# Kernel tuning notes

Measured on AMD Instinct MI355X. Metric: run time of the kernel, lower is better.

The kernel has to match this reference:

```python
import jax, jax.numpy as jnp
import numpy as np

B, C, H, W = 4, 256, 64, 64
DQ = C // 8

def setup_inputs() -> dict:
    key = jax.random.key(0)
    ks = jax.random.split(key, 7)
    x = jax.random.normal(ks[0], (B, C, H, W), dtype=jnp.float32)
    # 1x1 convs == per-pixel linear layers: weight [out, in], bias [out]
    Wq = jax.random.normal(ks[1], (DQ, C), dtype=jnp.float32) * (1.0 / np.sqrt(C))
    bq = jax.random.normal(ks[2], (DQ,), dtype=jnp.float32) * 0.01
    Wk = jax.random.normal(ks[3], (DQ, C), dtype=jnp.float32) * (1.0 / np.sqrt(C))
    bk = jax.random.normal(ks[4], (DQ,), dtype=jnp.float32) * 0.01
    Wv = jax.random.normal(ks[5], (C, C), dtype=jnp.float32) * (1.0 / np.sqrt(C))
    bv = jax.random.normal(ks[6], (C,), dtype=jnp.float32) * 0.01
    return {"x": x, "Wq": Wq, "bq": bq, "Wk": Wk, "bk": bk, "Wv": Wv, "bv": bv}

def reference(x, Wq, bq, Wk, bk, Wv, bv):
    b, c, h, w = x.shape
    n = h * w
    xf = x.reshape(b, c, n)                                  # [b,c,n]
    Q = jnp.einsum('dc,bcn->bnd', Wq, xf) + bq               # [b,n,dq]
    K = jnp.einsum('dc,bcn->bdn', Wk, xf) + bk[None, :, None]  # [b,dq,n]
    A = jax.nn.softmax(jnp.einsum('bnd,bdm->bnm', Q, K), axis=-1)  # [b,n,n]
    V = jnp.einsum('oc,bcn->bon', Wv, xf) + bv[None, :, None]      # [b,c,n]
    # torch: bmm(V, A^T) -> out[b,c,i] = sum_j V[b,c,j] * A[b,i,j]
    out = jnp.einsum('bcj,bij->bci', V, A)
    return x + out.reshape(b, c, h, w)
```

## Files before the change

kernel.cpp:

```cpp
#include <hip/hip_runtime.h>
#include <math.h>

#define BB 4
#define CC 256
#define NN 4096
#define DQ 32
#define LOG2E 1.44269504f

typedef _Float16 half8 __attribute__((ext_vector_type(8)));
typedef _Float16 half4 __attribute__((ext_vector_type(4)));
typedef float float4v __attribute__((ext_vector_type(4)));

__global__ __launch_bounds__(64) void prep_kernel(
    const float* __restrict__ Wq, const float* __restrict__ bq,
    const float* __restrict__ Wk, const float* __restrict__ bk,
    const float* __restrict__ Wv, const float* __restrict__ bv,
    _Float16* __restrict__ Wh, float* __restrict__ bh)
{
    int o = blockIdx.x, t = threadIdx.x;
    const float* src; float scale = 1.0f, bias;
    if (o < DQ)            { src = Wq + o * CC;        scale = LOG2E; bias = bq[o] * LOG2E; }
    else if (o < 2 * DQ)   { src = Wk + (o - DQ) * CC;                bias = bk[o - DQ]; }
    else                   { src = Wv + (o - 2 * DQ) * CC;            bias = bv[o - 2 * DQ]; }
    float4 v = *(const float4*)(src + t * 4);
    half4 h = { (_Float16)(v.x * scale), (_Float16)(v.y * scale),
                (_Float16)(v.z * scale), (_Float16)(v.w * scale) };
    *(half4*)(Wh + o * CC + t * 4) = h;
    if (t == 0) bh[o] = bias;
}

__global__ __launch_bounds__(256) void proj_kernel(
    const float* __restrict__ x, const _Float16* __restrict__ Wh,
    const float* __restrict__ bh,
    _Float16* __restrict__ Qt, _Float16* __restrict__ Kt,
    _Float16* __restrict__ Vh)
{
    __shared__ _Float16 xl[32 * 256];
    __shared__ _Float16 os_qk[32 * 72];
    __shared__ _Float16 os_v[256 * 40];

    const int tid = threadIdx.x;
    const int lane = tid & 63, w = tid >> 6;
    const int i16 = lane & 15, q = lane >> 4;
    const int n0 = blockIdx.x * 32, b = blockIdx.y;

    const float* xb = x + (size_t)b * CC * NN + n0;
    #pragma unroll
    for (int u = 0; u < 2; ++u) {
        int c0 = 4 * (tid >> 3) + 128 * u;
        int nn = 4 * (tid & 7);
        float4 rr[4];
        #pragma unroll
        for (int j = 0; j < 4; ++j)
            rr[j] = *(const float4*)(xb + (size_t)(c0 + j) * NN + nn);
        #pragma unroll
        for (int e = 0; e < 4; ++e) {
            int n = nn + e;
            half4 h = { (_Float16)((const float*)&rr[0])[e],
                        (_Float16)((const float*)&rr[1])[e],
                        (_Float16)((const float*)&rr[2])[e],
                        (_Float16)((const float*)&rr[3])[e] };
            int chunk = (c0 >> 3) ^ (n & 31);
            *(half4*)&xl[n * 256 + chunk * 8 + (c0 & 7)] = h;
        }
    }

    float4v acc[5][2];
    const int obase = 80 * w;
    #pragma unroll
    for (int ot = 0; ot < 5; ++ot) {
        float4 b4 = *(const float4*)(bh + obase + 16 * ot + 4 * q);
        #pragma unroll
        for (int nt = 0; nt < 2; ++nt)
            acc[ot][nt] = (float4v){b4.x, b4.y, b4.z, b4.w};
    }

    const _Float16* wbase = Wh + (size_t)(obase + i16) * CC + 8 * q;
    half8 afc[5];
    #pragma unroll
    for (int ot = 0; ot < 5; ++ot)
        afc[ot] = *(const half8*)(wbase + (size_t)16 * ot * CC);
    __syncthreads();

    #pragma unroll
    for (int k = 0; k < 8; ++k) {
        half8 afn[5];
        int kn = (k + 1) & 7;
        #pragma unroll
        for (int ot = 0; ot < 5; ++ot)
            afn[ot] = *(const half8*)(wbase + (size_t)16 * ot * CC + kn * 32);
        half8 bf[2];
        #pragma unroll
        for (int nt = 0; nt < 2; ++nt) {
            int n = 16 * nt + i16;
            bf[nt] = *(const half8*)&xl[n * 256 + (((4 * k + q) ^ (n & 31)) * 8)];
        }
        #pragma unroll
        for (int ot = 0; ot < 5; ++ot)
            #pragma unroll
            for (int nt = 0; nt < 2; ++nt)
                acc[ot][nt] = __builtin_amdgcn_mfma_f32_16x16x32_f16(afc[ot], bf[nt], acc[ot][nt], 0, 0, 0);
        #pragma unroll
        for (int ot = 0; ot < 5; ++ot)
            afc[ot] = afn[ot];
    }

    #pragma unroll
    for (int ot = 0; ot < 5; ++ot) {
        int og = obase + 16 * ot;
        #pragma unroll
        for (int nt = 0; nt < 2; ++nt) {
            int n = 16 * nt + i16;
            if (og < 64) {
                half4 hv = { (_Float16)acc[ot][nt][0], (_Float16)acc[ot][nt][1],
                             (_Float16)acc[ot][nt][2], (_Float16)acc[ot][nt][3] };
                *(half4*)&os_qk[n * 72 + og + 4 * q] = hv;
            } else {
                int cb = og - 64 + 4 * q;
                #pragma unroll
                for (int r = 0; r < 4; ++r)
                    os_v[(cb + r) * 40 + n] = (_Float16)acc[ot][nt][r];
            }
        }
    }
    __syncthreads();

    _Float16* Qtb = Qt + (size_t)b * NN * DQ;
    _Float16* Ktb = Kt + (size_t)b * NN * DQ;
    {
        int n = tid >> 3, p = tid & 7;
        half8 hv = *(const half8*)&os_qk[n * 72 + 8 * p];
        if (p < 4) *(half8*)(Qtb + (size_t)(n0 + n) * DQ + 8 * p) = hv;
        else       *(half8*)(Ktb + (size_t)(n0 + n) * DQ + 8 * (p - 4)) = hv;
    }
    _Float16* Vb = Vh + (size_t)b * CC * NN;
    #pragma unroll
    for (int u = 0; u < 4; ++u) {
        int c = u * 64 + (tid >> 2), p = tid & 3;
        half8 hv = *(const half8*)&os_v[c * 40 + 8 * p];
        *(half8*)(Vb + (size_t)c * NN + n0 + 8 * p) = hv;
    }
}

#define RS_TILE(KC, KN, U)                                                     \
    {                                                                          \
        const int un = ((U) + 1) & 15;                                         \
        _Pragma("unroll")                                                      \
        for (int jt = 0; jt < 4; ++jt)                                         \
            KN[jt] = *(const half8*)(kb0 + un * 64 * DQ + jt * 16 * DQ);       \
        _Pragma("unroll")                                                      \
        for (int jt = 0; jt < 4; ++jt) {                                       \
            float4v z = {0.f, 0.f, 0.f, 0.f};                                  \
            float4v s = __builtin_amdgcn_mfma_f32_16x16x32_f16(KC[jt], qb, z, 0, 0, 0); \
            l += exp2f(s[0]); l += exp2f(s[1]);                                \
            l += exp2f(s[2]); l += exp2f(s[3]);                                \
        }                                                                      \
    }

__global__ __launch_bounds__(256) void rowstat_kernel(
    const _Float16* __restrict__ Qt, const _Float16* __restrict__ Kt,
    float* __restrict__ L)
{
    const int tid = threadIdx.x;
    const int lane = tid & 63, w = tid >> 6;
    const int i16 = lane & 15, q = lane >> 4;
    const int q0 = blockIdx.x * 64, js = blockIdx.y, b = blockIdx.z;

    const _Float16* Qtb = Qt + (size_t)b * NN * DQ;
    const _Float16* Ktb = Kt + (size_t)b * NN * DQ;
    half8 qb = *(const half8*)(Qtb + (size_t)(q0 + 16 * w + i16) * DQ + 8 * q);
    const _Float16* kb0 = Ktb + (size_t)(js * 1024 + i16) * DQ + 8 * q;

    float l = 0.f;
    half8 kA[4], kB[4];
    #pragma unroll
    for (int jt = 0; jt < 4; ++jt)
        kA[jt] = *(const half8*)(kb0 + jt * 16 * DQ);
    for (int uu = 0; uu < 8; ++uu) {
        RS_TILE(kA, kB, 2 * uu);
        RS_TILE(kB, kA, 2 * uu + 1);
    }
    l += __shfl_xor(l, 16, 64);
    l += __shfl_xor(l, 32, 64);
    if (q == 0)
        L[((size_t)b * 4 + js) * NN + q0 + 16 * w + i16] = l;
}

#define STAGE_LOAD(TT)                                                          \
    {                                                                           \
        const int j0s = (TT) * 32;                                              \
        _Pragma("unroll")                                                       \
        for (int u = 0; u < 2; ++u) {                                           \
            int idx = u * 512 + tid;                                            \
            int c = idx >> 2, jc = idx & 3;                                     \
            gv[u] = *(const half8*)(Vb + (size_t)c * NN + j0s + jc * 8);        \
        }                                                                       \
        if (tid < 128) {                                                        \
            int j = tid >> 2, dc = tid & 3;                                     \
            gk = *(const half8*)(Ktb + (size_t)(j0s + j) * DQ + dc * 8);        \
        }                                                                       \
    }

#define STAGE_WRITE(BUF)                                                        \
    {                                                                           \
        _Pragma("unroll")                                                       \
        for (int u = 0; u < 2; ++u) {                                           \
            int idx = u * 512 + tid;                                            \
            int c = idx >> 2, jc = idx & 3;                                     \
            *(half8*)&v_lds[BUF][c * 32 + ((jc ^ (c & 3)) * 8)] = gv[u];        \
        }                                                                       \
        if (tid < 128) {                                                        \
            int j = tid >> 2, dc = tid & 3;                                     \
            *(half8*)&k_lds[BUF][j * 32 + ((dc ^ (j & 3)) * 8)] = gk;           \
        }                                                                       \
    }

__global__ __launch_bounds__(512) void attn_kernel(
    const float* __restrict__ x,
    const _Float16* __restrict__ Qt, const _Float16* __restrict__ Kt,
    const _Float16* __restrict__ Vh, const float* __restrict__ L,
    float* __restrict__ out)
{
    __shared__ _Float16 k_lds[2][32 * 32];
    __shared__ _Float16 v_lds[2][256 * 32];

    const int tid = threadIdx.x;
    const int w = tid >> 6, lane = tid & 63;
    const int i16 = lane & 15, q = lane >> 4;
    const int wq = w >> 2, wc = w & 3;
    const int id = blockIdx.x;
    const int b = (id & 7) >> 1;
    const int i0 = 64 * ((id >> 3) * 2 + (id & 1));
    const int qbase = i0 + 32 * wq;

    const _Float16* Ktb = Kt + (size_t)b * NN * DQ;
    const _Float16* Vb  = Vh + (size_t)b * CC * NN;

    float lg[2];
    #pragma unroll
    for (int it = 0; it < 2; ++it) {
        int qi = qbase + 16 * it + i16;
        float l = 0.f;
        #pragma unroll
        for (int js = 0; js < 4; ++js)
            l += L[((size_t)b * 4 + js) * NN + qi];
        lg[it] = log2f(l);
    }

    half8 qb[2];
    {
        const _Float16* Qtb = Qt + (size_t)b * NN * DQ;
        qb[0] = *(const half8*)(Qtb + (size_t)(qbase + i16) * DQ + 8 * q);
        qb[1] = *(const half8*)(Qtb + (size_t)(qbase + 16 + i16) * DQ + 8 * q);
    }

    float4v O[4][2];
    #pragma unroll
    for (int ct = 0; ct < 4; ++ct)
        #pragma unroll
        for (int it = 0; it < 2; ++it)
            O[ct][it] = (float4v){0.f, 0.f, 0.f, 0.f};

    half8 gv[2], gk;
    STAGE_LOAD(0);
    STAGE_WRITE(0);
    __syncthreads();

    for (int t = 0; t < NN / 32; ++t) {
        const int cur = t & 1;
        if (t < NN / 32 - 1) STAGE_LOAD(t + 1);

        half8 ka[2];
        #pragma unroll
        for (int jt = 0; jt < 2; ++jt) {
            int j = 16 * jt + i16;
            ka[jt] = *(const half8*)&k_lds[cur][j * 32 + ((q ^ (j & 3)) * 8)];
        }

        #pragma unroll
        for (int jt = 0; jt < 2; ++jt) {
            half4 pb[2];
            #pragma unroll
            for (int it = 0; it < 2; ++it) {
                float4v z = {0.f, 0.f, 0.f, 0.f};
                float4v s = __builtin_amdgcn_mfma_f32_16x16x32_f16(ka[jt], qb[it], z, 0, 0, 0);
                pb[it] = (half4){ (_Float16)exp2f(s[0] - lg[it]),
                                  (_Float16)exp2f(s[1] - lg[it]),
                                  (_Float16)exp2f(s[2] - lg[it]),
                                  (_Float16)exp2f(s[3] - lg[it]) };
            }
            #pragma unroll
            for (int ct = 0; ct < 4; ++ct) {
                int c = 64 * wc + 16 * ct + i16;
                int off = c * 32 + (((2 * jt + (q >> 1)) ^ (c & 3)) * 8) + (q & 1) * 4;
                half4 va = *(const half4*)&v_lds[cur][off];
                #pragma unroll
                for (int it = 0; it < 2; ++it)
                    O[ct][it] = __builtin_amdgcn_mfma_f32_16x16x16f16(va, pb[it], O[ct][it], 0, 0, 0);
            }
        }

        if (t < NN / 32 - 1) STAGE_WRITE((t + 1) & 1);
        __syncthreads();
    }

    const float* xb = x + (size_t)b * CC * NN;
    float* ob = out + (size_t)b * CC * NN;
    #pragma unroll
    for (int ct = 0; ct < 4; ++ct)
        #pragma unroll
        for (int it = 0; it < 2; ++it)
            #pragma unroll
            for (int r = 0; r < 4; ++r) {
                int c = 64 * wc + 16 * ct + 4 * q + r;
                size_t idx = (size_t)c * NN + qbase + 16 * it + i16;
                ob[idx] = xb[idx] + O[ct][it][r];
            }
}

extern "C" void kernel_launch(void* const* d_in, const int* in_sizes, int n_in,
                              void* d_out, int out_size, void* d_ws, size_t ws_size,
                              hipStream_t stream) {
    const float* x  = (const float*)d_in[0];
    const float* Wq = (const float*)d_in[1];
    const float* bq = (const float*)d_in[2];
    const float* Wk = (const float*)d_in[3];
    const float* bk = (const float*)d_in[4];
    const float* Wv = (const float*)d_in[5];
    const float* bv = (const float*)d_in[6];
    float* out = (float*)d_out;

    char* ws = (char*)d_ws;
    _Float16* Wh = (_Float16*)(ws);
    float*    bh = (float*)(ws + 163840);
    _Float16* Qt = (_Float16*)(ws + 262144);
    _Float16* Kt = (_Float16*)(ws + 1310720);
    _Float16* Vh = (_Float16*)(ws + 2359296);
    float*    L  = (float*)(ws + 10747904);

    prep_kernel<<<dim3(320), 64, 0, stream>>>(Wq, bq, Wk, bk, Wv, bv, Wh, bh);
    proj_kernel<<<dim3(NN / 32, BB), 256, 0, stream>>>(x, Wh, bh, Qt, Kt, Vh);
    rowstat_kernel<<<dim3(NN / 64, 4, BB), 256, 0, stream>>>(Qt, Kt, L);
    attn_kernel<<<dim3(256), 512, 0, stream>>>(x, Qt, Kt, Vh, L, out);
}
```

Baseline: 234.0 us.

## Split attention over key halves, stream K/V from global, add reduce kernel

The attention kernel now splits the key dimension into two halves across blocks, doubling the grid. Each block computes P in LDS per 32-key tile and reads K and V fragments straight from global memory with register prefetch, instead of staging them in LDS. One half writes fp32 partial outputs and the other writes fp16 partials, and a new reduce kernel adds both to x. The projection kernel also uses 16-column tiles to double its grid. This trades extra global traffic and a kernel launch for more parallelism, and rounds one partial to fp16.

```diff
diff --git a/kernel.cpp b/kernel.cpp
--- a/kernel.cpp
+++ b/kernel.cpp
@@ -35,20 +35,19 @@
     _Float16* __restrict__ Qt, _Float16* __restrict__ Kt,
     _Float16* __restrict__ Vh)
 {
-    __shared__ _Float16 xl[32 * 256];
-    __shared__ _Float16 os_qk[32 * 72];
-    __shared__ _Float16 os_v[256 * 40];
+    __shared__ _Float16 xl[16 * 256];
+    __shared__ _Float16 os_qk[16 * 72];
+    __shared__ _Float16 os_v[256 * 24];
 
     const int tid = threadIdx.x;
     const int lane = tid & 63, w = tid >> 6;
     const int i16 = lane & 15, q = lane >> 4;
-    const int n0 = blockIdx.x * 32, b = blockIdx.y;
+    const int n0 = blockIdx.x * 16, b = blockIdx.y;
 
     const float* xb = x + (size_t)b * CC * NN + n0;
-    #pragma unroll
-    for (int u = 0; u < 2; ++u) {
-        int c0 = 4 * (tid >> 3) + 128 * u;
-        int nn = 4 * (tid & 7);
+    {
+        int c0 = 4 * (tid >> 2);
+        int nn = 4 * (tid & 3);
         float4 rr[4];
         #pragma unroll
         for (int j = 0; j < 4; ++j)
@@ -60,19 +59,17 @@
                         (_Float16)((const float*)&rr[1])[e],
                         (_Float16)((const float*)&rr[2])[e],
                         (_Float16)((const float*)&rr[3])[e] };
-            int chunk = (c0 >> 3) ^ (n & 31);
+            int chunk = (c0 >> 3) ^ n;
             *(half4*)&xl[n * 256 + chunk * 8 + (c0 & 7)] = h;
         }
     }
 
-    float4v acc[5][2];
+    float4v acc[5];
     const int obase = 80 * w;
     #pragma unroll
     for (int ot = 0; ot < 5; ++ot) {
         float4 b4 = *(const float4*)(bh + obase + 16 * ot + 4 * q);
-        #pragma unroll
-        for (int nt = 0; nt < 2; ++nt)
-            acc[ot][nt] = (float4v){b4.x, b4.y, b4.z, b4.w};
+        acc[ot] = (float4v){b4.x, b4.y, b4.z, b4.w};
     }
 
     const _Float16* wbase = Wh + (size_t)(obase + i16) * CC + 8 * q;
@@ -89,17 +86,10 @@
         #pragma unroll
         for (int ot = 0; ot < 5; ++ot)
             afn[ot] = *(const half8*)(wbase + (size_t)16 * ot * CC + kn * 32);
-        half8 bf[2];
-        #pragma unroll
-        for (int nt = 0; nt < 2; ++nt) {
-            int n = 16 * nt + i16;
-            bf[nt] = *(const half8*)&xl[n * 256 + (((4 * k + q) ^ (n & 31)) * 8)];
-        }
+        half8 bf = *(const half8*)&xl[i16 * 256 + (((4 * k + q) ^ i16) * 8)];
         #pragma unroll
         for (int ot = 0; ot < 5; ++ot)
-            #pragma unroll
-            for (int nt = 0; nt < 2; ++nt)
-                acc[ot][nt] = __builtin_amdgcn_mfma_f32_16x16x32_f16(afc[ot], bf[nt], acc[ot][nt], 0, 0, 0);
+            acc[ot] = __builtin_amdgcn_mfma_f32_16x16x32_f16(afc[ot], bf, acc[ot], 0, 0, 0);
         #pragma unroll
         for (int ot = 0; ot < 5; ++ot)
             afc[ot] = afn[ot];
@@ -108,26 +98,22 @@
     #pragma unroll
     for (int ot = 0; ot < 5; ++ot) {
         int og = obase + 16 * ot;
-        #pragma unroll
-        for (int nt = 0; nt < 2; ++nt) {
-            int n = 16 * nt + i16;
-            if (og < 64) {
-                half4 hv = { (_Float16)acc[ot][nt][0], (_Float16)acc[ot][nt][1],
-                             (_Float16)acc[ot][nt][2], (_Float16)acc[ot][nt][3] };
-                *(half4*)&os_qk[n * 72 + og + 4 * q] = hv;
-            } else {
-                int cb = og - 64 + 4 * q;
-                #pragma unroll
-                for (int r = 0; r < 4; ++r)
-                    os_v[(cb + r) * 40 + n] = (_Float16)acc[ot][nt][r];
-            }
+        if (og < 64) {
+            half4 hv = { (_Float16)acc[ot][0], (_Float16)acc[ot][1],
+                         (_Float16)acc[ot][2], (_Float16)acc[ot][3] };
+            *(half4*)&os_qk[i16 * 72 + og + 4 * q] = hv;
+        } else {
+            int cb = og - 64 + 4 * q;
+            #pragma unroll
+            for (int r = 0; r < 4; ++r)
+                os_v[(cb + r) * 24 + i16] = (_Float16)acc[ot][r];
         }
     }
     __syncthreads();
 
     _Float16* Qtb = Qt + (size_t)b * NN * DQ;
     _Float16* Ktb = Kt + (size_t)b * NN * DQ;
-    {
+    if (tid < 128) {
         int n = tid >> 3, p = tid & 7;
         half8 hv = *(const half8*)&os_qk[n * 72 + 8 * p];
         if (p < 4) *(half8*)(Qtb + (size_t)(n0 + n) * DQ + 8 * p) = hv;
@@ -135,9 +121,9 @@
     }
     _Float16* Vb = Vh + (size_t)b * CC * NN;
     #pragma unroll
-    for (int u = 0; u < 4; ++u) {
-        int c = u * 64 + (tid >> 2), p = tid & 3;
-        half8 hv = *(const half8*)&os_v[c * 40 + 8 * p];
+    for (int u = 0; u < 2; ++u) {
+        int c = u * 128 + (tid >> 1), p = tid & 1;
+        half8 hv = *(const half8*)&os_v[c * 24 + 8 * p];
         *(half8*)(Vb + (size_t)c * NN + n0 + 8 * p) = hv;
     }
 }
@@ -186,136 +172,124 @@
         L[((size_t)b * 4 + js) * NN + q0 + 16 * w + i16] = l;
 }
 
-#define STAGE_LOAD(TT)                                                          \
-    {                                                                           \
-        const int j0s = (TT) * 32;                                              \
-        _Pragma("unroll")                                                       \
-        for (int u = 0; u < 2; ++u) {                                           \
-            int idx = u * 512 + tid;                                            \
-            int c = idx >> 2, jc = idx & 3;                                     \
-            gv[u] = *(const half8*)(Vb + (size_t)c * NN + j0s + jc * 8);        \
-        }                                                                       \
-        if (tid < 128) {                                                        \
-            int j = tid >> 2, dc = tid & 3;                                     \
-            gk = *(const half8*)(Ktb + (size_t)(j0s + j) * DQ + dc * 8);        \
-        }                                                                       \
-    }
-
-#define STAGE_WRITE(BUF)                                                        \
-    {                                                                           \
-        _Pragma("unroll")                                                       \
-        for (int u = 0; u < 2; ++u) {                                           \
-            int idx = u * 512 + tid;                                            \
-            int c = idx >> 2, jc = idx & 3;                                     \
-            *(half8*)&v_lds[BUF][c * 32 + ((jc ^ (c & 3)) * 8)] = gv[u];        \
-        }                                                                       \
-        if (tid < 128) {                                                        \
-            int j = tid >> 2, dc = tid & 3;                                     \
-            *(half8*)&k_lds[BUF][j * 32 + ((dc ^ (j & 3)) * 8)] = gk;           \
-        }                                                                       \
-    }
-
 __global__ __launch_bounds__(512) void attn_kernel(
-    const float* __restrict__ x,
     const _Float16* __restrict__ Qt, const _Float16* __restrict__ Kt,
     const _Float16* __restrict__ Vh, const float* __restrict__ L,
-    float* __restrict__ out)
-{
-    __shared__ _Float16 k_lds[2][32 * 32];
-    __shared__ _Float16 v_lds[2][256 * 32];
+    float* __restrict__ out, _Float16* __restrict__ Ph)
+{
+    __shared__ _Float16 pl[2][64 * 36];
 
     const int tid = threadIdx.x;
     const int w = tid >> 6, lane = tid & 63;
     const int i16 = lane & 15, q = lane >> 4;
-    const int wq = w >> 2, wc = w & 3;
+    const int itw = w & 3, jtw = w >> 2;
     const int id = blockIdx.x;
     const int b = (id & 7) >> 1;
-    const int i0 = 64 * ((id >> 3) * 2 + (id & 1));
-    const int qbase = i0 + 32 * wq;
-
-    const _Float16* Ktb = Kt + (size_t)b * NN * DQ;
-    const _Float16* Vb  = Vh + (size_t)b * CC * NN;
-
-    float lg[2];
-    #pragma unroll
-    for (int it = 0; it < 2; ++it) {
-        int qi = qbase + 16 * it + i16;
-        float l = 0.f;
+    const int ks = id & 1;
+    const int i0 = 64 * (id >> 3);
+    const int j00 = ks * 2048;
+
+    float4v lgs;
+    {
+        float4v s = {0.f, 0.f, 0.f, 0.f};
         #pragma unroll
         for (int js = 0; js < 4; ++js)
-            l += L[((size_t)b * 4 + js) * NN + qi];
-        lg[it] = log2f(l);
-    }
-
-    half8 qb[2];
-    {
-        const _Float16* Qtb = Qt + (size_t)b * NN * DQ;
-        qb[0] = *(const half8*)(Qtb + (size_t)(qbase + i16) * DQ + 8 * q);
-        qb[1] = *(const half8*)(Qtb + (size_t)(qbase + 16 + i16) * DQ + 8 * q);
-    }
+            s += *(const float4v*)(L + ((size_t)b * 4 + js) * NN + i0 + 16 * itw + 4 * q);
+        lgs[0] = log2f(s[0]); lgs[1] = log2f(s[1]);
+        lgs[2] = log2f(s[2]); lgs[3] = log2f(s[3]);
+    }
+
+    half8 qf = *(const half8*)(Qt + (size_t)b * NN * DQ
+                               + (size_t)(i0 + 16 * itw + i16) * DQ + 8 * q);
+
+    const _Float16* kptr = Kt + (size_t)b * NN * DQ
+                         + (size_t)(j00 + 16 * jtw + i16) * DQ + 8 * q;
+    const _Float16* vptr0 = Vh + (size_t)b * CC * NN
+                          + (size_t)(32 * w + i16) * NN + j00 + 8 * q;
+    const _Float16* vptr1 = vptr0 + (size_t)16 * NN;
 
     float4v O[4][2];
     #pragma unroll
-    for (int ct = 0; ct < 4; ++ct)
-        #pragma unroll
-        for (int it = 0; it < 2; ++it)
-            O[ct][it] = (float4v){0.f, 0.f, 0.f, 0.f};
-
-    half8 gv[2], gk;
-    STAGE_LOAD(0);
-    STAGE_WRITE(0);
-    __syncthreads();
-
-    for (int t = 0; t < NN / 32; ++t) {
-        const int cur = t & 1;
-        if (t < NN / 32 - 1) STAGE_LOAD(t + 1);
-
-        half8 ka[2];
-        #pragma unroll
-        for (int jt = 0; jt < 2; ++jt) {
-            int j = 16 * jt + i16;
-            ka[jt] = *(const half8*)&k_lds[cur][j * 32 + ((q ^ (j & 3)) * 8)];
-        }
-
-        #pragma unroll
-        for (int jt = 0; jt < 2; ++jt) {
-            half4 pb[2];
+    for (int it = 0; it < 4; ++it)
+        #pragma unroll
+        for (int ct = 0; ct < 2; ++ct)
+            O[it][ct] = (float4v){0.f, 0.f, 0.f, 0.f};
+
+    half8 kc, kn, vc0, vc1, vn0, vn1;
+    kc  = *(const half8*)kptr;
+    vc0 = *(const half8*)vptr0;
+    vc1 = *(const half8*)vptr1;
+
+    const int jcol = 16 * jtw + i16;
+
+    for (int t = 0; t < 64; ++t) {
+        if (t < 63) {
+            kn  = *(const half8*)(kptr + (size_t)(t + 1) * 32 * DQ);
+            vn0 = *(const half8*)(vptr0 + (t + 1) * 32);
+            vn1 = *(const half8*)(vptr1 + (t + 1) * 32);
+        }
+        _Float16* plb = &pl[t & 1][0];
+
+        {
+            float4v z = {0.f, 0.f, 0.f, 0.f};
+            float4v s = __builtin_amdgcn_mfma_f32_16x16x32_f16(qf, kc, z, 0, 0, 0);
             #pragma unroll
-            for (int it = 0; it < 2; ++it) {
-                float4v z = {0.f, 0.f, 0.f, 0.f};
-                float4v s = __builtin_amdgcn_mfma_f32_16x16x32_f16(ka[jt], qb[it], z, 0, 0, 0);
-                pb[it] = (half4){ (_Float16)exp2f(s[0] - lg[it]),
-                                  (_Float16)exp2f(s[1] - lg[it]),
-                                  (_Float16)exp2f(s[2] - lg[it]),
-                                  (_Float16)exp2f(s[3] - lg[it]) };
+            for (int r = 0; r < 4; ++r)
+                plb[(16 * itw + 4 * q + r) * 36 + jcol] = (_Float16)exp2f(s[r] - lgs[r]);
+        }
+        asm volatile("s_waitcnt lgkmcnt(0)\n\ts_barrier" ::: "memory");
+
+        half8 pa[4];
+        #pragma unroll
+        for (int it = 0; it < 4; ++it)
+            pa[it] = *(const half8*)&plb[(16 * it + i16) * 36 + 8 * q];
+        #pragma unroll
+        for (int it = 0; it < 4; ++it) {
+            O[it][0] = __builtin_amdgcn_mfma_f32_16x16x32_f16(pa[it], vc0, O[it][0], 0, 0, 0);
+            O[it][1] = __builtin_amdgcn_mfma_f32_16x16x32_f16(pa[it], vc1, O[it][1], 0, 0, 0);
+        }
+        kc = kn; vc0 = vn0; vc1 = vn1;
+    }
+
+    if (ks == 0) {
+        float* ob = out + (size_t)b * CC * NN;
+        #pragma unroll
+        for (int it = 0; it < 4; ++it)
+            #pragma unroll
+            for (int ct = 0; ct < 2; ++ct) {
+                int c = 32 * w + 16 * ct + i16;
+                *(float4v*)(ob + (size_t)c * NN + i0 + 16 * it + 4 * q) = O[it][ct];
             }
+    } else {
+        _Float16* pb = Ph + (size_t)b * CC * NN;
+        #pragma unroll
+        for (int it = 0; it < 4; ++it)
             #pragma unroll
-            for (int ct = 0; ct < 4; ++ct) {
-                int c = 64 * wc + 16 * ct + i16;
-                int off = c * 32 + (((2 * jt + (q >> 1)) ^ (c & 3)) * 8) + (q & 1) * 4;
-                half4 va = *(const half4*)&v_lds[cur][off];
-                #pragma unroll
-                for (int it = 0; it < 2; ++it)
-                    O[ct][it] = __builtin_amdgcn_mfma_f32_16x16x16f16(va, pb[it], O[ct][it], 0, 0, 0);
+            for (int ct = 0; ct < 2; ++ct) {
+                int c = 32 * w + 16 * ct + i16;
+                half4 hv = { (_Float16)O[it][ct][0], (_Float16)O[it][ct][1],
+                             (_Float16)O[it][ct][2], (_Float16)O[it][ct][3] };
+                *(half4*)(pb + (size_t)c * NN + i0 + 16 * it + 4 * q) = hv;
             }
-        }
-
-        if (t < NN / 32 - 1) STAGE_WRITE((t + 1) & 1);
-        __syncthreads();
-    }
-
-    const float* xb = x + (size_t)b * CC * NN;
-    float* ob = out + (size_t)b * CC * NN;
-    #pragma unroll
-    for (int ct = 0; ct < 4; ++ct)
-        #pragma unroll
-        for (int it = 0; it < 2; ++it)
-            #pragma unroll
-            for (int r = 0; r < 4; ++r) {
-                int c = 64 * wc + 16 * ct + 4 * q + r;
-                size_t idx = (size_t)c * NN + qbase + 16 * it + i16;
-                ob[idx] = xb[idx] + O[ct][it][r];
-            }
+    }
+}
+
+__global__ __launch_bounds__(256) void reduce_kernel(
+    const float* __restrict__ x, const _Float16* __restrict__ Ph,
+    float* __restrict__ out)
+{
+    size_t i8 = ((size_t)blockIdx.x * 256 + threadIdx.x) * 8;
+    float4 o0 = *(const float4*)(out + i8);
+    float4 o1 = *(const float4*)(out + i8 + 4);
+    float4 x0 = *(const float4*)(x + i8);
+    float4 x1 = *(const float4*)(x + i8 + 4);
+    half8 p = *(const half8*)(Ph + i8);
+    float4 r0 = { o0.x + x0.x + (float)p[0], o0.y + x0.y + (float)p[1],
+                  o0.z + x0.z + (float)p[2], o0.w + x0.w + (float)p[3] };
+    float4 r1 = { o1.x + x1.x + (float)p[4], o1.y + x1.y + (float)p[5],
+                  o1.z + x1.z + (float)p[6], o1.w + x1.w + (float)p[7] };
+    *(float4*)(out + i8) = r0;
+    *(float4*)(out + i8 + 4) = r1;
 }
 
 extern "C" void kernel_launch(void* const* d_in, const int* in_sizes, int n_in,
@@ -337,9 +311,11 @@
     _Float16* Kt = (_Float16*)(ws + 1310720);
     _Float16* Vh = (_Float16*)(ws + 2359296);
     float*    L  = (float*)(ws + 10747904);
+    _Float16* Ph = (_Float16*)(ws + 11010048);
 
     prep_kernel<<<dim3(320), 64, 0, stream>>>(Wq, bq, Wk, bk, Wv, bv, Wh, bh);
-    proj_kernel<<<dim3(NN / 32, BB), 256, 0, stream>>>(x, Wh, bh, Qt, Kt, Vh);
+    proj_kernel<<<dim3(NN / 16, BB), 256, 0, stream>>>(x, Wh, bh, Qt, Kt, Vh);
     rowstat_kernel<<<dim3(NN / 64, 4, BB), 256, 0, stream>>>(Qt, Kt, L);
-    attn_kernel<<<dim3(256), 512, 0, stream>>>(x, Qt, Kt, Vh, L, out);
-}
+    attn_kernel<<<dim3(512), 512, 0, stream>>>(Qt, Kt, Vh, L, out, Ph);
+    reduce_kernel<<<dim3((BB * CC * NN) / (256 * 8)), 256, 0, stream>>>(x, Ph, out);
+}
```

Measured after the change: 260.2 us. +11.2%, slower.
